# Kernel tuning notes

Measured on AMD Instinct MI355X. Metric: run time of the kernel, lower is better.

## Reference

```python
import jax, jax.numpy as jnp
import numpy as np

INPUT_CHANNELS = 64
OUT_CHANNELS = 64
OUT_DIM = 4
IN_FEAT = INPUT_CHANNELS * OUT_DIM * 2   # 512
OUT_FEAT = OUT_CHANNELS * OUT_DIM        # 256
BATCH = 65536


def setup_inputs() -> dict:
    key = jax.random.key(0)
    k_x, k_w, k_b = jax.random.split(key, 3)
    x = jax.random.normal(k_x, (BATCH, IN_FEAT), dtype=jnp.float32)
    weight = jax.random.normal(k_w, (OUT_FEAT, IN_FEAT), dtype=jnp.float32)
    bias = jax.random.normal(k_b, (1, OUT_FEAT), dtype=jnp.float32)
    return {"x": x, "weight": weight, "bias": bias}


def reference(x, weight, bias) -> jnp.ndarray:
    # Original: (x[:, None] * weight).sum(-1) / sqrt(input_channels) + 0.1*bias
    # Mathematically identical to a GEMM: x @ weight.T
    scale = 1.0 / jnp.sqrt(jnp.asarray(INPUT_CHANNELS, dtype=x.dtype))
    out = jnp.einsum('bi,oi->bo', x, weight) * scale  # [B, out_feat]
    out = out + bias * 0.1
    return out
```

## Files before the change

### kernel.cpp

```cpp
#include <hip/hip_runtime.h>
#include <hip/hip_bf16.h>


typedef __bf16 bf16;
typedef __attribute__((ext_vector_type(8))) __bf16 bf16x8;
typedef __attribute__((ext_vector_type(4))) __bf16 bf16x4;
typedef __attribute__((ext_vector_type(4))) float f32x4;

#define BATCH_ 65536
#define KDIM   512
#define NDIM   256

__global__ __launch_bounds__(256) void wcvt_kernel(const float* __restrict__ w,
                                                   bf16* __restrict__ wb) {
    int i = (blockIdx.x * 256 + threadIdx.x) * 4;
    f32x4 v = *(const f32x4*)(w + i);
    bf16x4 o;
    o[0] = (bf16)(v.x * 0.125f);
    o[1] = (bf16)(v.y * 0.125f);
    o[2] = (bf16)(v.z * 0.125f);
    o[3] = (bf16)(v.w * 0.125f);
    *(bf16x4*)(wb + i) = o;
}

__global__ __launch_bounds__(256) void gemm_kernel(const float* __restrict__ x,
                                                   const bf16* __restrict__ wb,
                                                   const float* __restrict__ bias,
                                                   float* __restrict__ out) {
    const int lane = threadIdx.x & 63;
    const int wv   = threadIdx.x >> 6;
    const int q    = lane >> 4;
    const int l16  = lane & 15;
    const long m0  = (long)blockIdx.x * 64;
    const int  n0  = wv * 64;

    const float* xp[4];
    const bf16*  wp[4];
#pragma unroll
    for (int t = 0; t < 4; ++t) {
        xp[t] = x  + (m0 + t * 16 + l16) * KDIM + q * 8;
        wp[t] = wb + (long)(n0 + t * 16 + l16) * KDIM + q * 8;
    }

    f32x4 acc[4][4];
#pragma unroll
    for (int i = 0; i < 4; ++i)
#pragma unroll
        for (int j = 0; j < 4; ++j)
            acc[i][j] = (f32x4)0.0f;

#pragma unroll 4
    for (int kc = 0; kc < 16; ++kc) {
        bf16x8 a[4], b[4];
#pragma unroll
        for (int mt = 0; mt < 4; ++mt) {
            f32x4 lo = *(const f32x4*)(xp[mt] + kc * 32);
            f32x4 hi = *(const f32x4*)(xp[mt] + kc * 32 + 4);
            bf16x8 av;
            av[0] = (bf16)lo.x; av[1] = (bf16)lo.y;
            av[2] = (bf16)lo.z; av[3] = (bf16)lo.w;
            av[4] = (bf16)hi.x; av[5] = (bf16)hi.y;
            av[6] = (bf16)hi.z; av[7] = (bf16)hi.w;
            a[mt] = av;
        }
#pragma unroll
        for (int nt = 0; nt < 4; ++nt)
            b[nt] = *(const bf16x8*)(wp[nt] + kc * 32);
#pragma unroll
        for (int mt = 0; mt < 4; ++mt)
#pragma unroll
            for (int nt = 0; nt < 4; ++nt)
                acc[mt][nt] = __builtin_amdgcn_mfma_f32_16x16x32_bf16(
                    a[mt], b[nt], acc[mt][nt], 0, 0, 0);
    }

    float bv[4];
#pragma unroll
    for (int nt = 0; nt < 4; ++nt)
        bv[nt] = 0.1f * bias[n0 + nt * 16 + l16];

#pragma unroll
    for (int mt = 0; mt < 4; ++mt)
#pragma unroll
        for (int nt = 0; nt < 4; ++nt)
#pragma unroll
            for (int r = 0; r < 4; ++r) {
                long row = m0 + mt * 16 + q * 4 + r;
                out[row * NDIM + n0 + nt * 16 + l16] = acc[mt][nt][r] + bv[nt];
            }
}

extern "C" void kernel_launch(void* const* d_in, const int* in_sizes, int n_in,
                              void* d_out, int out_size, void* d_ws, size_t ws_size,
                              hipStream_t stream) {
    const float* x    = (const float*)d_in[0];
    const float* w    = (const float*)d_in[1];
    const float* bias = (const float*)d_in[2];
    float* out = (float*)d_out;
    bf16* wb   = (bf16*)d_ws;

    wcvt_kernel<<<(NDIM * KDIM) / (256 * 4), 256, 0, stream>>>(w, wb);
    gemm_kernel<<<BATCH_ / 64, 256, 0, stream>>>(x, wb, bias, out);
}
```

Before: 267.6 us.

## Halve GEMM row tile, software-prefetch next K chunk, use nontemporal output stores

Cuts the per-block row tile from 64 to 32, doubling the grid, and sets launch bounds for 4 blocks per SIMD to raise occupancy. The K loop is fully unrolled and loads the next chunk's x and weight fragments while the current chunk's MFMAs run, to hide global memory latency. Output stores become nontemporal to avoid polluting cache with the streamed result. The full unroll with per-chunk register arrays risks high register pressure and spills. Because each wave now covers fewer rows, the weight fragments are reloaded more often per output row.

```diff
diff --git a/kernel.cpp b/kernel.cpp
--- a/kernel.cpp
+++ b/kernel.cpp
@@ -10,6 +10,8 @@
 #define BATCH_ 65536
 #define KDIM   512
 #define NDIM   256
+#define BM     32
+#define NCHUNK 16
 
 __global__ __launch_bounds__(256) void wcvt_kernel(const float* __restrict__ w,
                                                    bf16* __restrict__ wb) {
@@ -23,55 +25,74 @@
     *(bf16x4*)(wb + i) = o;
 }
 
-__global__ __launch_bounds__(256) void gemm_kernel(const float* __restrict__ x,
-                                                   const bf16* __restrict__ wb,
-                                                   const float* __restrict__ bias,
-                                                   float* __restrict__ out) {
+__device__ __forceinline__ bf16x8 cvt_a(f32x4 lo, f32x4 hi) {
+    bf16x8 a;
+    a[0] = (bf16)lo.x; a[1] = (bf16)lo.y; a[2] = (bf16)lo.z; a[3] = (bf16)lo.w;
+    a[4] = (bf16)hi.x; a[5] = (bf16)hi.y; a[6] = (bf16)hi.z; a[7] = (bf16)hi.w;
+    return a;
+}
+
+__global__ __launch_bounds__(256, 4) void gemm_kernel(const float* __restrict__ x,
+                                                      const bf16* __restrict__ wb,
+                                                      const float* __restrict__ bias,
+                                                      float* __restrict__ out) {
     const int lane = threadIdx.x & 63;
     const int wv   = threadIdx.x >> 6;
     const int q    = lane >> 4;
     const int l16  = lane & 15;
-    const long m0  = (long)blockIdx.x * 64;
+    const long m0  = (long)blockIdx.x * BM;
     const int  n0  = wv * 64;
 
-    const float* xp[4];
+    const float* xp[2];
     const bf16*  wp[4];
 #pragma unroll
-    for (int t = 0; t < 4; ++t) {
-        xp[t] = x  + (m0 + t * 16 + l16) * KDIM + q * 8;
+    for (int t = 0; t < 2; ++t)
+        xp[t] = x + (m0 + t * 16 + l16) * KDIM + q * 8;
+#pragma unroll
+    for (int t = 0; t < 4; ++t)
         wp[t] = wb + (long)(n0 + t * 16 + l16) * KDIM + q * 8;
-    }
 
-    f32x4 acc[4][4];
+    f32x4 acc[2][4];
 #pragma unroll
-    for (int i = 0; i < 4; ++i)
+    for (int i = 0; i < 2; ++i)
 #pragma unroll
         for (int j = 0; j < 4; ++j)
             acc[i][j] = (f32x4)0.0f;
 
-#pragma unroll 4
-    for (int kc = 0; kc < 16; ++kc) {
-        bf16x8 a[4], b[4];
+    f32x4 alo[NCHUNK][2], ahi[NCHUNK][2];
+    bf16x8 bfr[NCHUNK][4];
+
 #pragma unroll
-        for (int mt = 0; mt < 4; ++mt) {
-            f32x4 lo = *(const f32x4*)(xp[mt] + kc * 32);
-            f32x4 hi = *(const f32x4*)(xp[mt] + kc * 32 + 4);
-            bf16x8 av;
-            av[0] = (bf16)lo.x; av[1] = (bf16)lo.y;
-            av[2] = (bf16)lo.z; av[3] = (bf16)lo.w;
-            av[4] = (bf16)hi.x; av[5] = (bf16)hi.y;
-            av[6] = (bf16)hi.z; av[7] = (bf16)hi.w;
-            a[mt] = av;
+    for (int mt = 0; mt < 2; ++mt) {
+        alo[0][mt] = *(const f32x4*)(xp[mt]);
+        ahi[0][mt] = *(const f32x4*)(xp[mt] + 4);
+    }
+#pragma unroll
+    for (int nt = 0; nt < 4; ++nt)
+        bfr[0][nt] = *(const bf16x8*)(wp[nt]);
+
+#pragma unroll
+    for (int kc = 0; kc < NCHUNK; ++kc) {
+        if (kc + 1 < NCHUNK) {
+#pragma unroll
+            for (int mt = 0; mt < 2; ++mt) {
+                alo[kc + 1][mt] = *(const f32x4*)(xp[mt] + (kc + 1) * 32);
+                ahi[kc + 1][mt] = *(const f32x4*)(xp[mt] + (kc + 1) * 32 + 4);
+            }
+#pragma unroll
+            for (int nt = 0; nt < 4; ++nt)
+                bfr[kc + 1][nt] = *(const bf16x8*)(wp[nt] + (kc + 1) * 32);
         }
+        bf16x8 a[2];
 #pragma unroll
-        for (int nt = 0; nt < 4; ++nt)
-            b[nt] = *(const bf16x8*)(wp[nt] + kc * 32);
+        for (int mt = 0; mt < 2; ++mt)
+            a[mt] = cvt_a(alo[kc][mt], ahi[kc][mt]);
 #pragma unroll
-        for (int mt = 0; mt < 4; ++mt)
+        for (int mt = 0; mt < 2; ++mt)
 #pragma unroll
             for (int nt = 0; nt < 4; ++nt)
                 acc[mt][nt] = __builtin_amdgcn_mfma_f32_16x16x32_bf16(
-                    a[mt], b[nt], acc[mt][nt], 0, 0, 0);
+                    a[mt], bfr[kc][nt], acc[mt][nt], 0, 0, 0);
     }
 
     float bv[4];
@@ -80,13 +101,14 @@
         bv[nt] = 0.1f * bias[n0 + nt * 16 + l16];
 
 #pragma unroll
-    for (int mt = 0; mt < 4; ++mt)
+    for (int mt = 0; mt < 2; ++mt)
 #pragma unroll
         for (int nt = 0; nt < 4; ++nt)
 #pragma unroll
             for (int r = 0; r < 4; ++r) {
                 long row = m0 + mt * 16 + q * 4 + r;
-                out[row * NDIM + n0 + nt * 16 + l16] = acc[mt][nt][r] + bv[nt];
+                __builtin_nontemporal_store(acc[mt][nt][r] + bv[nt],
+                                            &out[row * NDIM + n0 + nt * 16 + l16]);
             }
 }
 
@@ -100,5 +122,5 @@
     bf16* wb   = (bf16*)d_ws;
 
     wcvt_kernel<<<(NDIM * KDIM) / (256 * 4), 256, 0, stream>>>(w, wb);
-    gemm_kernel<<<BATCH_ / 64, 256, 0, stream>>>(x, wb, bias, out);
+    gemm_kernel<<<BATCH_ / BM, 256, 0, stream>>>(x, wb, bias, out);
 }
```

Measured after the change: 293.5 us. 9.7% more time.

## Keep weight slice in registers and stream x through swizzled double-buffered LDS

Applied to the files above, without the earlier changes.

The GEMM is restructured so each wave holds its 16-column slice of the bf16 weights in registers for the whole block. Each block walks 256 rows of x in 32-row chunks, using coalesced fp32 loads that are converted to bf16 and staged in XOR-swizzled, double-buffered LDS. The next chunk is prefetched into registers while the current one is consumed. This targets the strided, per-wave redundant global loads of x and the repeated weight fetches. In exchange, each block covers only half of N, so x is read twice, and every chunk needs a block-wide barrier.

```diff
diff --git a/kernel.cpp b/kernel.cpp
--- a/kernel.cpp
+++ b/kernel.cpp
@@ -10,6 +10,11 @@
 #define BATCH_ 65536
 #define KDIM   512
 #define NDIM   256
+#define ROWS_PER_CHUNK   32
+#define CHUNKS_PER_BLOCK 8
+#define ROWS_PER_BLOCK   256
+#define BN_BLOCK 128
+#define BN_WAVE  16
 
 __global__ __launch_bounds__(256) void wcvt_kernel(const float* __restrict__ w,
                                                    bf16* __restrict__ wb) {
@@ -23,71 +28,88 @@
     *(bf16x4*)(wb + i) = o;
 }
 
-__global__ __launch_bounds__(256) void gemm_kernel(const float* __restrict__ x,
-                                                   const bf16* __restrict__ wb,
-                                                   const float* __restrict__ bias,
-                                                   float* __restrict__ out) {
-    const int lane = threadIdx.x & 63;
-    const int wv   = threadIdx.x >> 6;
+__global__ __launch_bounds__(512, 2) void gemm_kernel(const float* __restrict__ x,
+                                                      const bf16* __restrict__ wb,
+                                                      const float* __restrict__ bias,
+                                                      float* __restrict__ out) {
+    __shared__ __align__(16) char lds[2][32 * 1024];
+
+    const int tid  = threadIdx.x;
+    const int lane = tid & 63;
+    const int w    = tid >> 6;
     const int q    = lane >> 4;
     const int l16  = lane & 15;
-    const long m0  = (long)blockIdx.x * 64;
-    const int  n0  = wv * 64;
 
-    const float* xp[4];
-    const bf16*  wp[4];
+    const int  ng = blockIdx.x & 1;
+    const long mg = blockIdx.x >> 1;
+    const long row_base = mg * ROWS_PER_BLOCK;
+    const int  n0 = ng * BN_BLOCK + w * BN_WAVE;
+
+    bf16x8 wf[16];
 #pragma unroll
-    for (int t = 0; t < 4; ++t) {
-        xp[t] = x  + (m0 + t * 16 + l16) * KDIM + q * 8;
-        wp[t] = wb + (long)(n0 + t * 16 + l16) * KDIM + q * 8;
-    }
+    for (int kc = 0; kc < 16; ++kc)
+        wf[kc] = *(const bf16x8*)(wb + (long)(n0 + l16) * KDIM + kc * 32 + q * 8);
 
-    f32x4 acc[4][4];
+    const float bv = 0.1f * bias[n0 + l16];
+
+    const float* xw = x + (row_base + (long)w * 4) * KDIM + lane * 4;
+
+    f32x4 ld[8];
 #pragma unroll
-    for (int i = 0; i < 4; ++i)
+    for (int j = 0; j < 4; ++j)
 #pragma unroll
-        for (int j = 0; j < 4; ++j)
-            acc[i][j] = (f32x4)0.0f;
+        for (int h = 0; h < 2; ++h)
+            ld[j * 2 + h] = *(const f32x4*)(xw + (long)j * KDIM + h * 256);
 
-#pragma unroll 4
-    for (int kc = 0; kc < 16; ++kc) {
-        bf16x8 a[4], b[4];
-#pragma unroll
-        for (int mt = 0; mt < 4; ++mt) {
-            f32x4 lo = *(const f32x4*)(xp[mt] + kc * 32);
-            f32x4 hi = *(const f32x4*)(xp[mt] + kc * 32 + 4);
-            bf16x8 av;
-            av[0] = (bf16)lo.x; av[1] = (bf16)lo.y;
-            av[2] = (bf16)lo.z; av[3] = (bf16)lo.w;
-            av[4] = (bf16)hi.x; av[5] = (bf16)hi.y;
-            av[6] = (bf16)hi.z; av[7] = (bf16)hi.w;
-            a[mt] = av;
-        }
-#pragma unroll
-        for (int nt = 0; nt < 4; ++nt)
-            b[nt] = *(const bf16x8*)(wp[nt] + kc * 32);
-#pragma unroll
-        for (int mt = 0; mt < 4; ++mt)
-#pragma unroll
-            for (int nt = 0; nt < 4; ++nt)
-                acc[mt][nt] = __builtin_amdgcn_mfma_f32_16x16x32_bf16(
-                    a[mt], b[nt], acc[mt][nt], 0, 0, 0);
-    }
-
-    float bv[4];
-#pragma unroll
-    for (int nt = 0; nt < 4; ++nt)
-        bv[nt] = 0.1f * bias[n0 + nt * 16 + l16];
+    for (int t = 0; t < CHUNKS_PER_BLOCK; ++t) {
+        char* buf = lds[t & 1];
 
 #pragma unroll
-    for (int mt = 0; mt < 4; ++mt)
+        for (int j = 0; j < 4; ++j) {
+            const int rr = w * 4 + j;
 #pragma unroll
-        for (int nt = 0; nt < 4; ++nt)
+            for (int h = 0; h < 2; ++h) {
+                f32x4 v = ld[j * 2 + h];
+                bf16x4 o;
+                o[0] = (bf16)v.x; o[1] = (bf16)v.y;
+                o[2] = (bf16)v.z; o[3] = (bf16)v.w;
+                const int g  = h * 32 + (lane >> 1);
+                const int gs = g ^ (rr & 7);
+                *(bf16x4*)(buf + rr * 1024 + gs * 16 + (lane & 1) * 8) = o;
+            }
+        }
+
+        __syncthreads();
+
+        if (t + 1 < CHUNKS_PER_BLOCK) {
 #pragma unroll
-            for (int r = 0; r < 4; ++r) {
-                long row = m0 + mt * 16 + q * 4 + r;
-                out[row * NDIM + n0 + nt * 16 + l16] = acc[mt][nt][r] + bv[nt];
+            for (int j = 0; j < 4; ++j)
+#pragma unroll
+                for (int h = 0; h < 2; ++h)
+                    ld[j * 2 + h] = *(const f32x4*)(xw + ((long)(t + 1) * 32 + j) * KDIM + h * 256);
+        }
+
+        f32x4 acc[2];
+        acc[0] = (f32x4)0.0f;
+        acc[1] = (f32x4)0.0f;
+#pragma unroll
+        for (int kc = 0; kc < 16; ++kc) {
+#pragma unroll
+            for (int mt = 0; mt < 2; ++mt) {
+                const int rr = mt * 16 + l16;
+                const int gs = (kc * 4 + q) ^ (rr & 7);
+                bf16x8 a = *(const bf16x8*)(buf + rr * 1024 + gs * 16);
+                acc[mt] = __builtin_amdgcn_mfma_f32_16x16x32_bf16(a, wf[kc], acc[mt], 0, 0, 0);
             }
+        }
+
+        const long row0 = row_base + (long)t * ROWS_PER_CHUNK;
+#pragma unroll
+        for (int mt = 0; mt < 2; ++mt)
+#pragma unroll
+            for (int r = 0; r < 4; ++r)
+                out[(row0 + mt * 16 + q * 4 + r) * NDIM + n0 + l16] = acc[mt][r] + bv;
+    }
 }
 
 extern "C" void kernel_launch(void* const* d_in, const int* in_sizes, int n_in,
@@ -100,5 +122,5 @@
     bf16* wb   = (bf16*)d_ws;
 
     wcvt_kernel<<<(NDIM * KDIM) / (256 * 4), 256, 0, stream>>>(w, wb);
-    gemm_kernel<<<BATCH_ / 64, 256, 0, stream>>>(x, wb, bias, out);
+    gemm_kernel<<<(BATCH_ / ROWS_PER_BLOCK) * (NDIM / BN_BLOCK), 512, 0, stream>>>(x, wb, bias, out);
 }
```

New measurement: 233.9 us. 1.14x faster.
